# Kernel tuning notes

Measured on AMD Instinct MI355X. Metric: run time of the kernel, lower is better.

## Reference

```python
import jax, jax.numpy as jnp
import numpy as np

HID, H, P, N, G, K = 2688, 64, 64, 128, 8, 4
I = H * P            # intermediate_size = 4096
GN = G * N           # groups_ssm_state_size = 1024
CONV_DIM = I + 2 * GN  # 6144
TOTAL = 2 * I + 2 * GN + H  # 10304
EPS = 1e-5


def setup_inputs() -> dict:
    key = jax.random.key(0)
    ks = jax.random.split(key, 8)
    B, T = 2, 2048
    hidden_states = jax.random.normal(ks[0], (B, T, HID), dtype=jnp.float32)
    in_proj_w = jax.random.normal(ks[1], (TOTAL, HID), dtype=jnp.float32) * 0.02
    conv_w = jax.random.normal(ks[2], (CONV_DIM, K), dtype=jnp.float32) * 0.1  # depthwise kernel
    conv_b = jnp.zeros((CONV_DIM,), dtype=jnp.float32)
    A = -jnp.exp(jax.random.normal(ks[3], (H,), dtype=jnp.float32))
    D = jnp.ones((H,), dtype=jnp.float32)
    dt_bias = jnp.ones((H,), dtype=jnp.float32)
    norm_weight = jnp.ones((I,), dtype=jnp.float32)
    out_proj_w = jax.random.normal(ks[4], (HID, I), dtype=jnp.float32) * 0.02
    return {"hidden_states": hidden_states, "in_proj_w": in_proj_w, "conv_w": conv_w,
            "conv_b": conv_b, "A": A, "D": D, "dt_bias": dt_bias,
            "norm_weight": norm_weight, "out_proj_w": out_proj_w}


def reference(hidden_states, in_proj_w, conv_w, conv_b, A, D, dt_bias, norm_weight, out_proj_w):
    B, T, _ = hidden_states.shape
    hpg = H // G  # heads per group

    # 1-2. in_proj and split
    proj = jnp.einsum('bth,oh->bto', hidden_states, in_proj_w)  # (B,T,TOTAL)
    gate = proj[..., :I]
    xBC = proj[..., I:I + CONV_DIM]
    dt = proj[..., I + CONV_DIM:]  # (B,T,H)

    # 3. causal depthwise conv1d (left-pad K-1, slice to T) + silu
    xp = jnp.pad(xBC, ((0, 0), (K - 1, 0), (0, 0)))
    conv = conv_b
    for i in range(K):  # tiny fixed kernel loop
        conv = conv + xp[:, i:i + T, :] * conv_w[:, i]
    conv = jax.nn.silu(conv)

    # 4-5. split and reshape
    x = conv[..., :I].reshape(B, T, H, P)
    Bm = conv[..., I:I + GN].reshape(B, T, G, N)
    Cm = conv[..., I + GN:].reshape(B, T, G, N)

    # 6. selective scan (precompute dt / A_bar outside the scan)
    dt_sp = jax.nn.softplus(dt + dt_bias)          # (B,T,H)
    A_bar = jnp.exp(A * dt_sp)                     # (B,T,H)
    xg = x.reshape(B, T, G, hpg, P)
    Ab = A_bar.reshape(B, T, G, hpg)
    dts = dt_sp.reshape(B, T, G, hpg)

    def step(h, inp):
        x_t, B_t, C_t, Ab_t, dt_t = inp  # (B,G,hpg,P),(B,G,N),(B,G,N),(B,G,hpg),(B,G,hpg)
        outer = dt_t[..., None, None] * x_t[..., None] * B_t[:, :, None, None, :]
        h = Ab_t[..., None, None] * h + outer      # (B,G,hpg,P,N)
        y_t = jnp.einsum('bghpn,bgn->bghp', h, C_t)
        return h, y_t

    inputs = (jnp.moveaxis(xg, 1, 0), jnp.moveaxis(Bm, 1, 0), jnp.moveaxis(Cm, 1, 0),
              jnp.moveaxis(Ab, 1, 0), jnp.moveaxis(dts, 1, 0))
    h0 = jnp.zeros((B, G, hpg, P, N), dtype=hidden_states.dtype)
    _, ys = jax.lax.scan(step, h0, inputs)         # (T,B,G,hpg,P)
    y = jnp.moveaxis(ys, 0, 1).reshape(B, T, H, P) + D[None, None, :, None] * x
    y = y.reshape(B, T, I)

    # 7. gated RMSNorm
    y = y * jax.nn.silu(gate)
    var = jnp.mean(y * y, axis=-1, keepdims=True)
    y = y * jax.lax.rsqrt(var + EPS) * norm_weight

    # 8. out_proj
    return jnp.einsum('bti,oi->bto', y, out_proj_w)
```

## Files before the change

### kernel.cpp

```cpp
#include <hip/hip_runtime.h>
#include <stdint.h>

typedef unsigned short ushort_t;
typedef __attribute__((ext_vector_type(4))) float f32x4;
typedef __attribute__((ext_vector_type(2))) float f32x2;
typedef __attribute__((ext_vector_type(8))) __bf16 bf16x8;
typedef __attribute__((ext_vector_type(4))) unsigned short u16x4;
typedef __attribute__((ext_vector_type(8))) unsigned short u16x8;

#define DEV __device__ __forceinline__

DEV void gload_lds16(const void* g, void* l) {
  __builtin_amdgcn_global_load_lds(
      (const __attribute__((address_space(1))) uint32_t*)(uintptr_t)(g),
      (__attribute__((address_space(3))) uint32_t*)(uintptr_t)(l), 16, 0, 0);
}

DEV ushort_t f2bf(float f) {
  union { float f; uint32_t u; } x; x.f = f;
  x.u += 0x7fffu + ((x.u >> 16) & 1u);
  return (ushort_t)(x.u >> 16);
}

DEV float bf2f(ushort_t u) {
  union { uint32_t u; float f; } x; x.u = (uint32_t)u << 16; return x.f;
}

DEV float siluf(float x) { return x / (1.f + expf(-x)); }

#define BAR asm volatile("s_barrier" ::: "memory")
#define LGKM0 do { asm volatile("s_waitcnt lgkmcnt(0)" ::: "memory"); \
                   __builtin_amdgcn_sched_barrier(0); } while (0)
#define VMCNT(n) asm volatile("s_waitcnt vmcnt(" #n ")" ::: "memory")

__global__ __launch_bounds__(256) void fill_kernel(float* p, float v, int n) {
  int i = blockIdx.x * 256 + threadIdx.x;
  if (i < n) p[i] = v;
}

__global__ __launch_bounds__(256) void cvt_bf16_kernel(const float* __restrict__ src,
                                                       ushort_t* __restrict__ dst,
                                                       int n_src4, int n_dst4) {
  int i = blockIdx.x * 256 + threadIdx.x;
  if (i >= n_dst4) return;
  f32x4 v;
  if (i < n_src4) v = *(const f32x4*)(src + (size_t)i * 4);
  else { v.x = 0.f; v.y = 0.f; v.z = 0.f; v.w = 0.f; }
  u16x4 o;
  o.x = f2bf(v.x); o.y = f2bf(v.y); o.z = f2bf(v.z); o.w = f2bf(v.w);
  *(u16x4*)(dst + (size_t)i * 4) = o;
}


DEV void ld_a4(const unsigned char* ab2, int mgofs, int ck0, int ck1, bf16x8 (&af)[4][2]) {
#pragma unroll
  for (int mi = 0; mi < 4; ++mi) {
    const unsigned char* p = ab2 + (mgofs + mi * 16) * 128;
    af[mi][0] = *(const bf16x8*)(p + ck0);
    af[mi][1] = *(const bf16x8*)(p + ck1);
  }
}

DEV void ld_b2(const unsigned char* bb2, int npofs, int ck0, int ck1, bf16x8 (&bf)[2][2]) {
#pragma unroll
  for (int ni = 0; ni < 2; ++ni) {
    const unsigned char* p = bb2 + (npofs + ni * 16) * 128;
    bf[ni][0] = *(const bf16x8*)(p + ck0);
    bf[ni][1] = *(const bf16x8*)(p + ck1);
  }
}

DEV void mm16(f32x4 (&acc)[8][4], const bf16x8 (&af)[4][2], const bf16x8 (&bf)[2][2],
              int mb, int nb) {
  __builtin_amdgcn_s_setprio(1);
#pragma unroll
  for (int mi = 0; mi < 4; ++mi)
#pragma unroll
    for (int ni = 0; ni < 2; ++ni)
#pragma unroll
      for (int kk = 0; kk < 2; ++kk)
        acc[mb + mi][nb + ni] = __builtin_amdgcn_mfma_f32_16x16x32_bf16(
            af[mi][kk], bf[ni][kk], acc[mb + mi][nb + ni], 0, 0, 0);
  __builtin_amdgcn_s_setprio(0);
}

DEV void stage2(const ushort_t* s0, const ushort_t* s1, unsigned char* d) {
  gload_lds16(s0, d);
  gload_lds16(s1, d + 8192);
}

template <int MODE>
__global__ __launch_bounds__(512, 1) void gemm8_kernel(const ushort_t* __restrict__ A,
                                                       const ushort_t* __restrict__ B,
                                                       void* __restrict__ C0,
                                                       void* __restrict__ C1,
                                                       int K, int NB, int NC, int niter) {
  __shared__ __align__(16) unsigned char lds[131072];
  const int tid = threadIdx.x;
  const int l = tid & 63, w = tid >> 6;
  const int wr = w >> 2, wc = w & 3;
  const int lr = l & 15, lk = l >> 4;
  const int xm = (lr & 7) << 4;
  const int ck0 = (lk * 16) ^ xm;
  const int ck1 = (64 + lk * 16) ^ xm;
  const int bm = blockIdx.x, bn = blockIdx.y;

  const int rr = (w << 3) + (l >> 3);
  const int cE = ((l & 7) ^ (l >> 3)) << 3;
  const int dstoff = w * 1024 + l * 16;

  const ushort_t* sA00 = A + (size_t)(bm * 256 +       rr) * K + cE;
  const ushort_t* sA01 = A + (size_t)(bm * 256 +  64 + rr) * K + cE;
  const ushort_t* sA10 = A + (size_t)(bm * 256 + 128 + rr) * K + cE;
  const ushort_t* sA11 = A + (size_t)(bm * 256 + 192 + rr) * K + cE;
  int rb0 = bn * 256 +       rr; if (rb0 > NB - 1) rb0 = NB - 1;
  int rb1 = bn * 256 +  64 + rr; if (rb1 > NB - 1) rb1 = NB - 1;
  int rb2 = bn * 256 + 128 + rr; if (rb2 > NB - 1) rb2 = NB - 1;
  int rb3 = bn * 256 + 192 + rr; if (rb3 > NB - 1) rb3 = NB - 1;
  const ushort_t* sB00 = B + (size_t)rb0 * K + cE;
  const ushort_t* sB01 = B + (size_t)rb1 * K + cE;
  const ushort_t* sB10 = B + (size_t)rb2 * K + cE;
  const ushort_t* sB11 = B + (size_t)rb3 * K + cE;

  const int aoff = wr * 16384 + lr * 128;
  const int boff = 32768 + (wc >> 1) * 16384 + ((wc & 1) * 64 + lr) * 128;

  f32x4 acc[8][4] = {};
  bf16x8 af[4][2], bf[2][2], bg[2][2];

  stage2(sA00, sA01, lds + dstoff);
  stage2(sA10, sA11, lds + 16384 + dstoff);
  stage2(sB00, sB01, lds + 32768 + dstoff);
  stage2(sB10, sB11, lds + 49152 + dstoff);
  stage2(sA00 + 64, sA01 + 64, lds + 65536 + dstoff);
  VMCNT(2);
  BAR;

  auto kpair = [&](int kt0, bool last) {
    const unsigned char* a0 = lds + aoff;
    const unsigned char* b0 = lds + boff;
    const unsigned char* a1 = lds + 65536 + aoff;
    const unsigned char* b1 = lds + 65536 + boff;
    const size_t c1 = (size_t)(kt0 + 1) * 64;
    const size_t c2 = (size_t)(kt0 + 2) * 64;
    const size_t c3 = (size_t)(kt0 + 3) * 64;
    ld_a4(a0, 0, ck0, ck1, af);
    ld_b2(b0, 0, ck0, ck1, bf);
    stage2(sA10 + c1, sA11 + c1, lds + 65536 + 16384 + dstoff);
    BAR; LGKM0; mm16(acc, af, bf, 0, 0); BAR;
    ld_b2(b0, 32, ck0, ck1, bg);
    stage2(sB00 + c1, sB01 + c1, lds + 65536 + 32768 + dstoff);
    BAR; LGKM0; mm16(acc, af, bg, 0, 2); BAR;
    ld_a4(a0, 64, ck0, ck1, af);
    stage2(sB10 + c1, sB11 + c1, lds + 65536 + 49152 + dstoff);
    BAR; LGKM0; mm16(acc, af, bg, 4, 2); BAR;
    ld_b2(b0, 0, ck0, ck1, bf);
    if (!last) { stage2(sA00 + c2, sA01 + c2, lds + dstoff); VMCNT(2); }
    else       { VMCNT(0); }
    BAR; LGKM0; mm16(acc, af, bf, 4, 0); BAR;
    ld_a4(a1, 0, ck0, ck1, af);
    ld_b2(b1, 0, ck0, ck1, bf);
    if (!last) stage2(sA10 + c2, sA11 + c2, lds + 16384 + dstoff);
    BAR; LGKM0; mm16(acc, af, bf, 0, 0); BAR;
    ld_b2(b1, 32, ck0, ck1, bg);
    if (!last) stage2(sB00 + c2, sB01 + c2, lds + 32768 + dstoff);
    BAR; LGKM0; mm16(acc, af, bg, 0, 2); BAR;
    ld_a4(a1, 64, ck0, ck1, af);
    if (!last) stage2(sB10 + c2, sB11 + c2, lds + 49152 + dstoff);
    BAR; LGKM0; mm16(acc, af, bg, 4, 2); BAR;
    ld_b2(b1, 0, ck0, ck1, bf);
    if (!last) { stage2(sA00 + c3, sA01 + c3, lds + 65536 + dstoff); VMCNT(2); }
    BAR; LGKM0; mm16(acc, af, bf, 4, 0); BAR;
  };

  for (int it = 0; it < niter - 1; ++it) kpair(2 * it, false);
  kpair(2 * (niter - 1), true);

  const int crow0 = bm * 256 + wr * 128 + (lk << 2);
  const int ccol0 = bn * 256 + wc * 64 + lr;
  if (MODE == 0) {
    ushort_t* gate = (ushort_t*)C0;
    ushort_t* xbc  = (ushort_t*)C1;
#pragma unroll
    for (int ni = 0; ni < 4; ++ni) {
      const int col = ccol0 + ni * 16;
      if (col < NC) {
        ushort_t* dst; size_t stride;
        if (col < 4096) { dst = gate + col; stride = 4096; }
        else            { dst = xbc + (col - 4096); stride = 6272; }
#pragma unroll
        for (int mi = 0; mi < 8; ++mi)
#pragma unroll
          for (int r = 0; r < 4; ++r)
            dst[(size_t)(crow0 + mi * 16 + r) * stride] = f2bf(acc[mi][ni][r]);
      }
    }
  } else {
    float* o = (float*)C0;
#pragma unroll
    for (int ni = 0; ni < 4; ++ni) {
      const int col = ccol0 + ni * 16;
      if (col < NC) {
#pragma unroll
        for (int mi = 0; mi < 8; ++mi)
#pragma unroll
          for (int r = 0; r < 4; ++r)
            o[(size_t)(crow0 + mi * 16 + r) * NC + col] = acc[mi][ni][r];
      }
    }
  }
}

__global__ __launch_bounds__(256) void conv_silu_kernel(const ushort_t* __restrict__ xbc,
                                                        const float* __restrict__ cw,
                                                        const float* __restrict__ cb,
                                                        ushort_t* __restrict__ out) {
  int idx = blockIdx.x * 256 + threadIdx.x;
  int c4 = (idx % 1536) << 2;
  int bt = idx / 1536;
  int t = bt & 2047;
  const ushort_t* base = xbc + (size_t)bt * 6272 + c4;
  f32x4 w0 = *(const f32x4*)&cw[(c4 + 0) * 4];
  f32x4 w1 = *(const f32x4*)&cw[(c4 + 1) * 4];
  f32x4 w2 = *(const f32x4*)&cw[(c4 + 2) * 4];
  f32x4 w3 = *(const f32x4*)&cw[(c4 + 3) * 4];
  f32x4 acc = *(const f32x4*)&cb[c4];
#pragma unroll
  for (int i = 0; i < 4; ++i) {
    int dt_ = i - 3;
    if (t + dt_ >= 0) {
      u16x4 xv = *(const u16x4*)(base + (ptrdiff_t)dt_ * 6272);
      acc.x += bf2f(xv.x) * w0[i];
      acc.y += bf2f(xv.y) * w1[i];
      acc.z += bf2f(xv.z) * w2[i];
      acc.w += bf2f(xv.w) * w3[i];
    }
  }
  u16x4 o;
  o.x = f2bf(siluf(acc.x)); o.y = f2bf(siluf(acc.y));
  o.z = f2bf(siluf(acc.z)); o.w = f2bf(siluf(acc.w));
  *(u16x4*)(out + (size_t)bt * 6144 + c4) = o;
}

__global__ __launch_bounds__(256) void dt_kernel(const ushort_t* __restrict__ xbc,
                                                 const float* __restrict__ dt_bias,
                                                 const float* __restrict__ Avec,
                                                 float* __restrict__ dtA) {
  int idx = blockIdx.x * 256 + threadIdx.x;
  int h = idx >> 12, bt = idx & 4095;
  float v = bf2f(xbc[(size_t)bt * 6272 + 6144 + h]) + dt_bias[h];
  float sp = fmaxf(v, 0.f) + log1pf(expf(-fabsf(v)));
  float ab = expf(Avec[h] * sp);
  dtA[(h << 13) + bt] = sp;
  dtA[(h << 13) + 4096 + bt] = ab;
}

template <int EMIT>
__global__ __launch_bounds__(256) void scan_chunk_kernel(const ushort_t* __restrict__ conv,
                                                         const float* __restrict__ dtA,
                                                         const float* __restrict__ Dvec,
                                                         const float* __restrict__ Avec,
                                                         ushort_t* __restrict__ yssm,
                                                         ushort_t* __restrict__ hst,
                                                         float* __restrict__ abprod) {
  const int bid = blockIdx.x;
  const int ck = bid & 7;
  const int ph = (bid >> 3) & 1;
  const int h = (bid >> 4) & 63;
  const int b = bid >> 10;
  const int g = h >> 3;
  const int tid = threadIdx.x;
  const int lane = tid & 63;
  const int wave = tid >> 6;
  const int pg = tid & 15, ng = tid >> 4;
  const int p0 = pg << 1, n0 = ng << 3;

  __shared__ __align__(16) unsigned char sraw[2][4672];
  __shared__ __align__(16) float ypart[2][4][8][32];

  const int btbase = (b << 11) + (ck << 8);
  const float* dt0 = dtA + (h << 13) + btbase;
  const float* dt1 = dt0 + 4096;
  const float Dh = Dvec[h];
  const int xcol = (h << 6) + (ph << 5);
  const size_t hbase = (size_t)bid * 4096;

  auto stage = [&](int tb) {
    unsigned char* dst = sraw[tb & 1];
    const int t0 = tb << 3;
    const size_t row0 = (size_t)(btbase + t0) * 6144;
#pragma unroll
    for (int j = 0; j < 2; ++j) {
      int c = tid + (j << 8);
      if (c < 292) {
        const void* src;
        if (c < 32)       { src = conv + row0 + (size_t)(c >> 2) * 6144 + xcol + ((c & 3) << 3); }
        else if (c < 160) { int r = c - 32;  src = conv + row0 + (size_t)(r >> 4) * 6144 + 4096 + (g << 7) + ((r & 15) << 3); }
        else if (c < 288) { int r = c - 160; src = conv + row0 + (size_t)(r >> 4) * 6144 + 5120 + (g << 7) + ((r & 15) << 3); }
        else if (c < 290) { src = dt0 + t0 + ((c - 288) << 2); }
        else              { src = dt1 + t0 + ((c - 290) << 2); }
        gload_lds16(src, dst + ((size_t)c << 4));
      }
    }
  };

  stage(0);

  float hs0[8], hs1[8];
  if (EMIT) {
    u16x8 a0 = *(const u16x8*)&hst[hbase + (size_t)p0 * 128 + n0];
    u16x8 a1 = *(const u16x8*)&hst[hbase + (size_t)(p0 + 1) * 128 + n0];
#pragma unroll
    for (int n = 0; n < 8; ++n) { hs0[n] = bf2f(a0[n]); hs1[n] = bf2f(a1[n]); }
  } else {
#pragma unroll
    for (int n = 0; n < 8; ++n) { hs0[n] = 0.f; hs1[n] = 0.f; }
  }
  float dtsum = 0.f;

  for (int tb = 0; tb < 32; ++tb) {
    __syncthreads();
    if (EMIT && tb > 0) {
      const int cur = (tb - 1) & 1;
      const int tprev = btbase + ((tb - 1) << 3);
      const int tt = tid >> 5, p = tid & 31;
      float v = ypart[cur][0][tt][p] + ypart[cur][1][tt][p] +
                ypart[cur][2][tt][p] + ypart[cur][3][tt][p];
      yssm[(size_t)(tprev + tt) * 4096 + xcol + p] = f2bf(v);
    }
    if (tb + 1 < 32) stage(tb + 1);
    const ushort_t* sbu = (const ushort_t*)sraw[tb & 1];
    const float* sfs = (const float*)(sraw[tb & 1] + 4608);
    const int cur = tb & 1;
#pragma unroll
    for (int tt = 0; tt < 8; ++tt) {
      uint32_t xv = *(const uint32_t*)&sbu[(tt << 5) + p0];
      float x0 = bf2f((ushort_t)xv), x1 = bf2f((ushort_t)(xv >> 16));
      u16x8 bv = *(const u16x8*)&sbu[256 + (tt << 7) + n0];
      float dtv = sfs[tt], ab = sfs[8 + tt];
      if (!EMIT) dtsum += dtv;
      float dtx0 = dtv * x0, dtx1 = dtv * x1;
      if (EMIT) {
        u16x8 cv = *(const u16x8*)&sbu[1280 + (tt << 7) + n0];
        float ys0 = 0.f, ys1 = 0.f;
#pragma unroll
        for (int n = 0; n < 8; ++n) {
          float Bn = bf2f(bv[n]), Cn = bf2f(cv[n]);
          hs0[n] = ab * hs0[n] + dtx0 * Bn; ys0 += hs0[n] * Cn;
          hs1[n] = ab * hs1[n] + dtx1 * Bn; ys1 += hs1[n] * Cn;
        }
        ys0 += __shfl_xor(ys0, 16, 64); ys0 += __shfl_xor(ys0, 32, 64);
        ys1 += __shfl_xor(ys1, 16, 64); ys1 += __shfl_xor(ys1, 32, 64);
        if (wave == 0) { ys0 += Dh * x0; ys1 += Dh * x1; }
        if ((lane >> 4) == 0) {
          f32x2 o; o.x = ys0; o.y = ys1;
          *(f32x2*)&ypart[cur][wave][tt][p0] = o;
        }
      } else {
#pragma unroll
        for (int n = 0; n < 8; ++n) {
          float Bn = bf2f(bv[n]);
          hs0[n] = ab * hs0[n] + dtx0 * Bn;
          hs1[n] = ab * hs1[n] + dtx1 * Bn;
        }
      }
    }
  }
  if (EMIT) {
    __syncthreads();
    const int cur = 31 & 1;
    const int tprev = btbase + (31 << 3);
    const int tt = tid >> 5, p = tid & 31;
    float v = ypart[cur][0][tt][p] + ypart[cur][1][tt][p] +
              ypart[cur][2][tt][p] + ypart[cur][3][tt][p];
    yssm[(size_t)(tprev + tt) * 4096 + xcol + p] = f2bf(v);
  } else {
    u16x8 o0, o1;
#pragma unroll
    for (int n = 0; n < 8; ++n) { o0[n] = f2bf(hs0[n]); o1[n] = f2bf(hs1[n]); }
    *(u16x8*)&hst[hbase + (size_t)p0 * 128 + n0] = o0;
    *(u16x8*)&hst[hbase + (size_t)(p0 + 1) * 128 + n0] = o1;
    if (ph == 0 && tid == 0)
      abprod[((b << 6) + h) * 8 + ck] = expf(Avec[h] * dtsum);
  }
}

__global__ __launch_bounds__(256) void combine_kernel(ushort_t* __restrict__ hst,
                                                      const float* __restrict__ abprod) {
  const int bid = blockIdx.x;
  const int bh = bid >> 1;
  const int tid = threadIdx.x;
  const size_t base = (size_t)bid * 8 * 4096 + tid * 16;
  float hrun[16];
#pragma unroll
  for (int e = 0; e < 16; ++e) hrun[e] = 0.f;
  for (int c = 0; c < 8; ++c) {
    const size_t p = base + (size_t)c * 4096;
    u16x8 v0 = *(const u16x8*)&hst[p];
    u16x8 v1 = *(const u16x8*)&hst[p + 8];
    float ab = abprod[bh * 8 + c];
    u16x8 w0, w1;
#pragma unroll
    for (int e = 0; e < 8; ++e) { w0[e] = f2bf(hrun[e]); w1[e] = f2bf(hrun[8 + e]); }
    *(u16x8*)&hst[p] = w0;
    *(u16x8*)&hst[p + 8] = w1;
#pragma unroll
    for (int e = 0; e < 8; ++e) {
      hrun[e] = ab * hrun[e] + bf2f(v0[e]);
      hrun[8 + e] = ab * hrun[8 + e] + bf2f(v1[e]);
    }
  }
}

__global__ __launch_bounds__(256) void norm_kernel(const ushort_t* __restrict__ yssm,
                                                   const ushort_t* __restrict__ gate,
                                                   const float* __restrict__ nw,
                                                   ushort_t* __restrict__ out) {
  const int bt = blockIdx.x;
  const int tid = threadIdx.x;
  const ushort_t* y = yssm + (size_t)bt * 4096;
  const ushort_t* gt = gate + (size_t)bt * 4096;
  float vals[16];
  float ss = 0.f;
#pragma unroll
  for (int j = 0; j < 4; ++j) {
    int o = (tid + j * 256) << 2;
    u16x4 yv = *(const u16x4*)(y + o);
    u16x4 gv = *(const u16x4*)(gt + o);
#pragma unroll
    for (int e = 0; e < 4; ++e) {
      float v = bf2f(yv[e]) * siluf(bf2f(gv[e]));
      vals[j * 4 + e] = v;
      ss += v * v;
    }
  }
#pragma unroll
  for (int m = 1; m <= 32; m <<= 1) ss += __shfl_xor(ss, m, 64);
  __shared__ float red[4];
  if ((tid & 63) == 0) red[tid >> 6] = ss;
  __syncthreads();
  ss = red[0] + red[1] + red[2] + red[3];
  const float sc = rsqrtf(ss * (1.f / 4096.f) + 1e-5f);
#pragma unroll
  for (int j = 0; j < 4; ++j) {
    int o = (tid + j * 256) << 2;
    f32x4 wv = *(const f32x4*)(nw + o);
    u16x4 ov;
    ov.x = f2bf(vals[j * 4 + 0] * sc * wv.x);
    ov.y = f2bf(vals[j * 4 + 1] * sc * wv.y);
    ov.z = f2bf(vals[j * 4 + 2] * sc * wv.z);
    ov.w = f2bf(vals[j * 4 + 3] * sc * wv.w);
    *(u16x4*)(out + (size_t)bt * 4096 + o) = ov;
  }
}

extern "C" void kernel_launch(void* const* d_in, const int* in_sizes, int n_in,
                              void* d_out, int out_size, void* d_ws, size_t ws_size,
                              hipStream_t stream) {
  const float* hidden  = (const float*)d_in[0];
  const float* w_in    = (const float*)d_in[1];
  const float* conv_w  = (const float*)d_in[2];
  const float* conv_b  = (const float*)d_in[3];
  const float* Avec    = (const float*)d_in[4];
  const float* Dvec    = (const float*)d_in[5];
  const float* dt_bias = (const float*)d_in[6];
  const float* nw      = (const float*)d_in[7];
  const float* w_out   = (const float*)d_in[8];
  float* out = (float*)d_out;

  char* ws = (char*)d_ws;
  ushort_t* Xbf   = (ushort_t*)(ws);
  ushort_t* W1bf  = (ushort_t*)(ws + 22020096);
  ushort_t* gate  = (ushort_t*)(ws + 77758464);
  ushort_t* xbc   = (ushort_t*)(ws + 111312896);
  ushort_t* W2bf  = Xbf;
  ushort_t* convb = W1bf;
  float*    dtA   = (float*)(ws + 22020096 + 50331648);
  float*    abprod= (float*)(ws + 22020096 + 52428800);
  ushort_t* yssm  = xbc;
  ushort_t* hst   = (ushort_t*)(ws + 111312896 + 33554432);
  ushort_t* ynorm = convb;
  const size_t NEED = 162693120;
  if (NEED > ws_size) {
    fill_kernel<<<4, 256, 0, stream>>>(out, 12345.0f, 1024);
    return;
  }

  cvt_bf16_kernel<<<10752, 256, 0, stream>>>(hidden, Xbf, 2752512, 2752512);
  cvt_bf16_kernel<<<27216, 256, 0, stream>>>(w_in, W1bf, 6924288, 6967296);
  gemm8_kernel<0><<<dim3(16, 41), 512, 0, stream>>>(Xbf, W1bf, gate, xbc,
                                                    2688, 10368, 10304, 21);
  cvt_bf16_kernel<<<10752, 256, 0, stream>>>(w_out, W2bf, 2752512, 2752512);
  conv_silu_kernel<<<24576, 256, 0, stream>>>(xbc, conv_w, conv_b, convb);
  dt_kernel<<<1024, 256, 0, stream>>>(xbc, dt_bias, Avec, dtA);
  scan_chunk_kernel<0><<<2048, 256, 0, stream>>>(convb, dtA, Dvec, Avec, yssm, hst, abprod);
  combine_kernel<<<256, 256, 0, stream>>>(hst, abprod);
  scan_chunk_kernel<1><<<2048, 256, 0, stream>>>(convb, dtA, Dvec, Avec, yssm, hst, abprod);
  norm_kernel<<<4096, 256, 0, stream>>>(yssm, gate, nw, ynorm);
  gemm8_kernel<1><<<dim3(16, 11), 512, 0, stream>>>(ynorm, W2bf, out, nullptr,
                                                    4096, 2688, 2688, 32);
}
```

Before: 812.9 us.

## Replace second sequential scan pass with MFMA-based inter-chunk state correction

The first scan pass now emits intra-chunk outputs (computed with zero initial state) along with the chunk end states. The second full sequential scan is replaced by a correction kernel that adds C_t · h_init scaled by the cumulative decay, computed as a small bf16 MFMA matmul per chunk. This removes a second pass of the serial recurrence over all timesteps. In exchange it adds a read-modify-write of yssm and an extra bf16 rounding of the partial outputs, which may cost some accuracy.

```diff
diff --git a/kernel.cpp b/kernel.cpp
--- a/kernel.cpp
+++ b/kernel.cpp
@@ -50,7 +50,6 @@
   o.x = f2bf(v.x); o.y = f2bf(v.y); o.z = f2bf(v.z); o.w = f2bf(v.w);
   *(u16x4*)(dst + (size_t)i * 4) = o;
 }
-
 
 DEV void ld_a4(const unsigned char* ab2, int mgofs, int ck0, int ck1, bf16x8 (&af)[4][2]) {
 #pragma unroll
@@ -255,8 +254,7 @@
   dtA[(h << 13) + 4096 + bt] = ab;
 }
 
-template <int EMIT>
-__global__ __launch_bounds__(256) void scan_chunk_kernel(const ushort_t* __restrict__ conv,
+__global__ __launch_bounds__(256) void scan_pass1_kernel(const ushort_t* __restrict__ conv,
                                                          const float* __restrict__ dtA,
                                                          const float* __restrict__ Dvec,
                                                          const float* __restrict__ Avec,
@@ -307,20 +305,13 @@
   stage(0);
 
   float hs0[8], hs1[8];
-  if (EMIT) {
-    u16x8 a0 = *(const u16x8*)&hst[hbase + (size_t)p0 * 128 + n0];
-    u16x8 a1 = *(const u16x8*)&hst[hbase + (size_t)(p0 + 1) * 128 + n0];
-#pragma unroll
-    for (int n = 0; n < 8; ++n) { hs0[n] = bf2f(a0[n]); hs1[n] = bf2f(a1[n]); }
-  } else {
-#pragma unroll
-    for (int n = 0; n < 8; ++n) { hs0[n] = 0.f; hs1[n] = 0.f; }
-  }
+#pragma unroll
+  for (int n = 0; n < 8; ++n) { hs0[n] = 0.f; hs1[n] = 0.f; }
   float dtsum = 0.f;
 
   for (int tb = 0; tb < 32; ++tb) {
     __syncthreads();
-    if (EMIT && tb > 0) {
+    if (tb > 0) {
       const int cur = (tb - 1) & 1;
       const int tprev = btbase + ((tb - 1) << 3);
       const int tt = tid >> 5, p = tid & 31;
@@ -337,51 +328,43 @@
       uint32_t xv = *(const uint32_t*)&sbu[(tt << 5) + p0];
       float x0 = bf2f((ushort_t)xv), x1 = bf2f((ushort_t)(xv >> 16));
       u16x8 bv = *(const u16x8*)&sbu[256 + (tt << 7) + n0];
+      u16x8 cv = *(const u16x8*)&sbu[1280 + (tt << 7) + n0];
       float dtv = sfs[tt], ab = sfs[8 + tt];
-      if (!EMIT) dtsum += dtv;
+      dtsum += dtv;
       float dtx0 = dtv * x0, dtx1 = dtv * x1;
-      if (EMIT) {
-        u16x8 cv = *(const u16x8*)&sbu[1280 + (tt << 7) + n0];
-        float ys0 = 0.f, ys1 = 0.f;
-#pragma unroll
-        for (int n = 0; n < 8; ++n) {
-          float Bn = bf2f(bv[n]), Cn = bf2f(cv[n]);
-          hs0[n] = ab * hs0[n] + dtx0 * Bn; ys0 += hs0[n] * Cn;
-          hs1[n] = ab * hs1[n] + dtx1 * Bn; ys1 += hs1[n] * Cn;
-        }
-        ys0 += __shfl_xor(ys0, 16, 64); ys0 += __shfl_xor(ys0, 32, 64);
-        ys1 += __shfl_xor(ys1, 16, 64); ys1 += __shfl_xor(ys1, 32, 64);
-        if (wave == 0) { ys0 += Dh * x0; ys1 += Dh * x1; }
-        if ((lane >> 4) == 0) {
-          f32x2 o; o.x = ys0; o.y = ys1;
-          *(f32x2*)&ypart[cur][wave][tt][p0] = o;
-        }
-      } else {
-#pragma unroll
-        for (int n = 0; n < 8; ++n) {
-          float Bn = bf2f(bv[n]);
-          hs0[n] = ab * hs0[n] + dtx0 * Bn;
-          hs1[n] = ab * hs1[n] + dtx1 * Bn;
-        }
+      float ys0 = 0.f, ys1 = 0.f;
+#pragma unroll
+      for (int n = 0; n < 8; ++n) {
+        float Bn = bf2f(bv[n]), Cn = bf2f(cv[n]);
+        hs0[n] = ab * hs0[n] + dtx0 * Bn; ys0 += hs0[n] * Cn;
+        hs1[n] = ab * hs1[n] + dtx1 * Bn; ys1 += hs1[n] * Cn;
       }
-    }
-  }
-  if (EMIT) {
-    __syncthreads();
+      ys0 += __shfl_xor(ys0, 16, 64); ys0 += __shfl_xor(ys0, 32, 64);
+      ys1 += __shfl_xor(ys1, 16, 64); ys1 += __shfl_xor(ys1, 32, 64);
+      if (wave == 0) { ys0 += Dh * x0; ys1 += Dh * x1; }
+      if ((lane >> 4) == 0) {
+        f32x2 o; o.x = ys0; o.y = ys1;
+        *(f32x2*)&ypart[cur][wave][tt][p0] = o;
+      }
+    }
+  }
+  {
+    u16x8 o0, o1;
+#pragma unroll
+    for (int n = 0; n < 8; ++n) { o0[n] = f2bf(hs0[n]); o1[n] = f2bf(hs1[n]); }
+    *(u16x8*)&hst[hbase + (size_t)p0 * 128 + n0] = o0;
+    *(u16x8*)&hst[hbase + (size_t)(p0 + 1) * 128 + n0] = o1;
+    if (ph == 0 && tid == 0)
+      abprod[((b << 6) + h) * 8 + ck] = expf(Avec[h] * dtsum);
+  }
+  __syncthreads();
+  {
     const int cur = 31 & 1;
     const int tprev = btbase + (31 << 3);
     const int tt = tid >> 5, p = tid & 31;
     float v = ypart[cur][0][tt][p] + ypart[cur][1][tt][p] +
               ypart[cur][2][tt][p] + ypart[cur][3][tt][p];
     yssm[(size_t)(tprev + tt) * 4096 + xcol + p] = f2bf(v);
-  } else {
-    u16x8 o0, o1;
-#pragma unroll
-    for (int n = 0; n < 8; ++n) { o0[n] = f2bf(hs0[n]); o1[n] = f2bf(hs1[n]); }
-    *(u16x8*)&hst[hbase + (size_t)p0 * 128 + n0] = o0;
-    *(u16x8*)&hst[hbase + (size_t)(p0 + 1) * 128 + n0] = o1;
-    if (ph == 0 && tid == 0)
-      abprod[((b << 6) + h) * 8 + ck] = expf(Avec[h] * dtsum);
   }
 }
 
@@ -408,6 +391,82 @@
     for (int e = 0; e < 8; ++e) {
       hrun[e] = ab * hrun[e] + bf2f(v0[e]);
       hrun[8 + e] = ab * hrun[8 + e] + bf2f(v1[e]);
+    }
+  }
+}
+
+__global__ __launch_bounds__(256) void correct_kernel(const ushort_t* __restrict__ conv,
+                                                      const float* __restrict__ dtA,
+                                                      const float* __restrict__ Avec,
+                                                      const ushort_t* __restrict__ hst,
+                                                      ushort_t* __restrict__ yssm) {
+  const int bid = blockIdx.x;
+  const int ck = bid & 7;
+  const int h = (bid >> 3) & 63;
+  const int b = bid >> 9;
+  const int g = h >> 3;
+  const int tid = threadIdx.x;
+  const int lane = tid & 63;
+  const int w = tid >> 6;
+  const int lr = lane & 15, lk = lane >> 4;
+  const int btb = (b << 11) + (ck << 8);
+
+  __shared__ float pdl[256];
+  __shared__ float wsum[4];
+  float s = dtA[(h << 13) + btb + tid];
+#pragma unroll
+  for (int off = 1; off < 64; off <<= 1) {
+    float t = __shfl_up(s, off, 64);
+    if (lane >= off) s += t;
+  }
+  if (lane == 63) wsum[w] = s;
+  __syncthreads();
+  float basev = 0.f;
+  for (int i = 0; i < w; ++i) basev += wsum[i];
+  pdl[tid] = expf(Avec[h] * (basev + s));
+  __syncthreads();
+
+  const ushort_t* Cc = conv + (size_t)btb * 6144 + 5120 + (g << 7);
+  const size_t hb0 = ((size_t)((b << 10) | (h << 4) | (0 << 3) | ck)) * 4096;
+  const size_t hb1 = ((size_t)((b << 10) | (h << 4) | (1 << 3) | ck)) * 4096;
+
+  f32x4 acc[4][4] = {};
+#pragma unroll
+  for (int kk = 0; kk < 4; ++kk) {
+    const int k0 = kk * 32 + lk * 8;
+    bf16x8 afr[4], bfr[4];
+#pragma unroll
+    for (int mf = 0; mf < 4; ++mf) {
+      const int t = w * 64 + mf * 16 + lr;
+      afr[mf] = *(const bf16x8*)(Cc + (size_t)t * 6144 + k0);
+    }
+#pragma unroll
+    for (int nf = 0; nf < 4; ++nf) {
+      const int p = nf * 16 + lr;
+      const size_t hb = (p < 32) ? hb0 : hb1;
+      bfr[nf] = *(const bf16x8*)(hst + hb + (size_t)(p & 31) * 128 + k0);
+    }
+#pragma unroll
+    for (int mf = 0; mf < 4; ++mf)
+#pragma unroll
+      for (int nf = 0; nf < 4; ++nf)
+        acc[mf][nf] = __builtin_amdgcn_mfma_f32_16x16x32_bf16(afr[mf], bfr[nf],
+                                                              acc[mf][nf], 0, 0, 0);
+  }
+
+#pragma unroll
+  for (int mf = 0; mf < 4; ++mf) {
+#pragma unroll
+    for (int r = 0; r < 4; ++r) {
+      const int row = w * 64 + mf * 16 + (lk << 2) + r;
+      const float pd = pdl[row];
+      const size_t yrow = (size_t)(btb + row) * 4096 + (h << 6);
+#pragma unroll
+      for (int nf = 0; nf < 4; ++nf) {
+        const int p = nf * 16 + lr;
+        const size_t idx = yrow + p;
+        yssm[idx] = f2bf(bf2f(yssm[idx]) + pd * acc[mf][nf][r]);
+      }
     }
   }
 }
@@ -493,9 +552,9 @@
   cvt_bf16_kernel<<<10752, 256, 0, stream>>>(w_out, W2bf, 2752512, 2752512);
   conv_silu_kernel<<<24576, 256, 0, stream>>>(xbc, conv_w, conv_b, convb);
   dt_kernel<<<1024, 256, 0, stream>>>(xbc, dt_bias, Avec, dtA);
-  scan_chunk_kernel<0><<<2048, 256, 0, stream>>>(convb, dtA, Dvec, Avec, yssm, hst, abprod);
+  scan_pass1_kernel<<<2048, 256, 0, stream>>>(convb, dtA, Dvec, Avec, yssm, hst, abprod);
   combine_kernel<<<256, 256, 0, stream>>>(hst, abprod);
-  scan_chunk_kernel<1><<<2048, 256, 0, stream>>>(convb, dtA, Dvec, Avec, yssm, hst, abprod);
+  correct_kernel<<<1024, 256, 0, stream>>>(convb, dtA, Avec, hst, yssm);
   norm_kernel<<<4096, 256, 0, stream>>>(yssm, gate, nw, ynorm);
   gemm8_kernel<1><<<dim3(16, 11), 512, 0, stream>>>(ynorm, W2bf, out, nullptr,
                                                     4096, 2688, 2688, 32);
```

Result: faster. 789.9 us (-2.8%).
